# Optimization experiments

Measured on AMD Instinct MI355X. Metric: run time of the kernel, lower is better.

The kernel has to match this reference:

```python
import jax, jax.numpy as jnp
import numpy as np

BSZ, SEQ, EMBED = 2, 4096, 1024
NUM_HEADS = 16
HEAD_DIM = EMBED // NUM_HEADS
WINDOW = 256  # attention_window[layer_id]


def setup_inputs() -> dict:
    key = jax.random.key(0)
    ks = jax.random.split(key, 7)
    s = 1.0 / np.sqrt(EMBED)
    return {
        "hidden_states": jax.random.normal(ks[0], (BSZ, SEQ, EMBED), jnp.float32),
        "Wq": jax.random.normal(ks[1], (EMBED, EMBED), jnp.float32) * s,
        "bq": jnp.zeros((EMBED,), jnp.float32),
        "Wk": jax.random.normal(ks[2], (EMBED, EMBED), jnp.float32) * s,
        "bk": jnp.zeros((EMBED,), jnp.float32),
        "Wv": jax.random.normal(ks[3], (EMBED, EMBED), jnp.float32) * s,
        "bv": jnp.zeros((EMBED,), jnp.float32),
    }


def _blocks3(x, nb, w):
    # x: [b, s + 2w, h, d] -> [b, nb, 3w, h, d]; block c sees key blocks c-1, c, c+1
    b = x.shape[0]
    xb = x.reshape(b, nb + 2, w, NUM_HEADS, HEAD_DIM)
    return jnp.concatenate([xb[:, i:i + nb] for i in range(3)], axis=2)


def reference(hidden_states, Wq, bq, Wk, bk, Wv, bv):
    b, s, e = hidden_states.shape
    w = WINDOW
    nb = s // w
    q = (hidden_states @ Wq + bq) * (1.0 / np.sqrt(HEAD_DIM))
    k = hidden_states @ Wk + bk
    v = hidden_states @ Wv + bv
    q = q.reshape(b, nb, w, NUM_HEADS, HEAD_DIM)
    k = k.reshape(b, s, NUM_HEADS, HEAD_DIM)
    v = v.reshape(b, s, NUM_HEADS, HEAD_DIM)
    pad = ((0, 0), (w, w), (0, 0), (0, 0))
    kb = _blocks3(jnp.pad(k, pad), nb, w)  # [b, nb, 3w, h, d]
    vb = _blocks3(jnp.pad(v, pad), nb, w)
    # banded scores: query x in block n attends keys at global pos n*w - w + y
    scores = jnp.einsum('bnxhd,bnyhd->bnhxy', q, kb)  # [b, nb, h, w, 3w]
    x_idx = jnp.arange(w)
    y_idx = jnp.arange(3 * w)
    band = jnp.abs(y_idx[None, :] - x_idx[:, None] - w) <= w  # [w, 3w]
    kpos = jnp.arange(nb)[:, None] * w - w + y_idx[None, :]   # [nb, 3w]
    inb = (kpos >= 0) & (kpos < s)
    mask = band[None, :, :] & inb[:, None, :]                 # [nb, w, 3w]
    scores = jnp.where(mask[None, :, None, :, :], scores, -jnp.inf)
    probs = jax.nn.softmax(scores.astype(jnp.float32), axis=-1).astype(v.dtype)
    attn = jnp.einsum('bnhxy,bnyhd->bnxhd', probs, vb)        # [b, nb, w, h, d]
    return attn.reshape(b, s, e)
```

## Files before the change

### kernel.cpp

```cpp
#include <hip/hip_runtime.h>
#include <stdint.h>

#define SEQ    4096
#define EMBED  1024
#define NHEAD  16
#define HDIM   64
#define WIN    256
#define BSZ    2
#define M_TOT  (BSZ * SEQ)
#define N_QKV  3072
#define N_QK   2048
#define K_DIM  1024
#define LOG2E  1.4426950408889634f

typedef __attribute__((ext_vector_type(8))) __bf16 bf16x8;
typedef __attribute__((ext_vector_type(4))) float  f32x4;

__device__ __forceinline__ unsigned short f2bf(float f) {
  union { float f; unsigned int u; } c; c.f = f;
  unsigned int u = c.u;
  unsigned int r = (u + 0x7FFFu + ((u >> 16) & 1u)) >> 16;
  return (unsigned short)r;
}

__device__ __forceinline__ unsigned int cvt_pk_bf16(float lo, float hi) {
  unsigned int r;
  asm("v_cvt_pk_bf16_f32 %0, %1, %2" : "=v"(r) : "v"(lo), "v"(hi));
  return r;
}

__device__ __forceinline__ void gl2lds16(const void* g, void* l) {
  __builtin_amdgcn_global_load_lds((const __attribute__((address_space(1))) void*)g,
                                   (__attribute__((address_space(3))) void*)l, 16, 0, 0);
}

__global__ __launch_bounds__(256) void cvt_all(const float* __restrict__ in,
                                               unsigned short* __restrict__ out,
                                               const float* __restrict__ Wq,
                                               const float* __restrict__ Wk,
                                               const float* __restrict__ Wv,
                                               unsigned short* __restrict__ Wt) {
  __shared__ float t[32][33];
  int tid = threadIdx.x;
  if (blockIdx.x < 8192) {
    int i = (blockIdx.x * 256 + tid) * 4;
    float4 v = *(const float4*)(in + i);
    ushort4 o;
    o.x = f2bf(v.x); o.y = f2bf(v.y); o.z = f2bf(v.z); o.w = f2bf(v.w);
    *(ushort4*)(out + i) = o;
  } else {
    int wb = blockIdx.x - 8192;
    int z  = wb >> 10;
    int rem = wb & 1023;
    int kb = (rem & 31) * 32, nb = (rem >> 5) * 32;
    const float* W = (z == 0) ? Wq : (z == 1) ? Wk : Wv;
    int tx = tid & 31, ty = tid >> 5;
    for (int it = 0; it < 4; ++it) {
      int k = kb + ty + it * 8;
      t[ty + it * 8][tx] = W[(size_t)k * 1024 + nb + tx];
    }
    __syncthreads();
    for (int it = 0; it < 4; ++it) {
      int n = nb + ty + it * 8;
      Wt[(size_t)(z * 1024 + n) * 1024 + kb + tx] = f2bf(t[tx][ty + it * 8]);
    }
  }
}

__global__ __launch_bounds__(512, 2) void qkv_gemm(const unsigned short* __restrict__ A,
                                                   const unsigned short* __restrict__ Bt,
                                                   const float* __restrict__ bq,
                                                   const float* __restrict__ bk,
                                                   const float* __restrict__ bv,
                                                   unsigned short* __restrict__ C,
                                                   unsigned short* __restrict__ Vt) {
  __shared__ unsigned short As[2][128 * 64];
  __shared__ unsigned short Bs[2][384 * 64];
  int tid  = threadIdx.x;
  int lane = tid & 63, wave = tid >> 6;
  int ln   = lane & 15, quad = lane >> 4;
  int flat = blockIdx.y * 8 + blockIdx.x;
  int swz  = (flat & 7) * 64 + (flat >> 3);
  int m0 = (swz >> 3) * 128, n0 = (swz & 7) * 384;
  int wy = wave >> 2, wx = wave & 3;
  f32x4 acc[4][6];
#pragma unroll
  for (int i = 0; i < 4; ++i)
#pragma unroll
    for (int j = 0; j < 6; ++j) acc[i][j] = (f32x4){0.f, 0.f, 0.f, 0.f};

  int c8 = tid & 7;

#define STG_A(buf, kt)                                                           \
  do {                                                                           \
    _Pragma("unroll")                                                            \
    for (int s = 0; s < 2; ++s) {                                                \
      int r = s * 64 + (tid >> 3); int cg = c8 ^ (r & 7);                        \
      gl2lds16(A + (size_t)(m0 + r) * K_DIM + (size_t)(kt) * 64 + cg * 8,        \
               &As[buf][r * 64 + c8 * 8]);                                       \
    }                                                                            \
  } while (0)
#define STG_B(buf, jreg, kt)                                                     \
  do {                                                                           \
    _Pragma("unroll")                                                            \
    for (int s = 0; s < 2; ++s) {                                                \
      int r = s * 64 + (tid >> 3); int gr = (jreg) * 128 + r;                    \
      int cg = c8 ^ (gr & 7);                                                    \
      gl2lds16(Bt + (size_t)(n0 + gr) * K_DIM + (size_t)(kt) * 64 + cg * 8,      \
               &Bs[buf][gr * 64 + c8 * 8]);                                      \
    }                                                                            \
  } while (0)

  STG_A(0, 0); STG_B(0, 0, 0); STG_B(0, 1, 0); STG_B(0, 2, 0);
  STG_B(1, 0, 1); STG_B(1, 1, 1); STG_B(1, 2, 1);
  asm volatile("s_waitcnt vmcnt(6)" ::: "memory");
  __builtin_amdgcn_s_barrier();

  int aBase = wy * 64, bBase = wx * 96;

#pragma unroll 1
  for (int t = 0; t < 16; ++t) {
    int cur = t & 1;
    const unsigned short* as = As[cur];
    const unsigned short* bs = Bs[cur];
    bf16x8 af[4][2], bf01[2][2], bf23[2][2], bf45[2][2];

#pragma unroll
    for (int i2 = 0; i2 < 4; ++i2) {
      int row = aBase + i2 * 16 + ln;
#pragma unroll
      for (int ks = 0; ks < 2; ++ks) {
        int c = (ks * 4 + quad) ^ (row & 7);
        af[i2][ks] = *(const bf16x8*)&as[row * 64 + c * 8];
      }
    }
#pragma unroll
    for (int j2 = 0; j2 < 2; ++j2) {
      int row = bBase + j2 * 16 + ln;
#pragma unroll
      for (int ks = 0; ks < 2; ++ks) {
        int c = (ks * 4 + quad) ^ (row & 7);
        bf01[j2][ks] = *(const bf16x8*)&bs[row * 64 + c * 8];
      }
    }
    if (t < 15) STG_A(cur ^ 1, t + 1);
    __builtin_amdgcn_s_barrier();
    __builtin_amdgcn_s_setprio(1);
#pragma unroll
    for (int ks = 0; ks < 2; ++ks)
#pragma unroll
      for (int i2 = 0; i2 < 4; ++i2)
#pragma unroll
        for (int j2 = 0; j2 < 2; ++j2)
          acc[i2][j2] = __builtin_amdgcn_mfma_f32_16x16x32_bf16(af[i2][ks], bf01[j2][ks], acc[i2][j2], 0, 0, 0);
    __builtin_amdgcn_s_setprio(0);
    __builtin_amdgcn_s_barrier();

#pragma unroll
    for (int j2 = 0; j2 < 2; ++j2) {
      int row = bBase + 32 + j2 * 16 + ln;
#pragma unroll
      for (int ks = 0; ks < 2; ++ks) {
        int c = (ks * 4 + quad) ^ (row & 7);
        bf23[j2][ks] = *(const bf16x8*)&bs[row * 64 + c * 8];
      }
    }
    __builtin_amdgcn_s_barrier();
    __builtin_amdgcn_s_setprio(1);
#pragma unroll
    for (int ks = 0; ks < 2; ++ks)
#pragma unroll
      for (int i2 = 0; i2 < 4; ++i2)
#pragma unroll
        for (int j2 = 0; j2 < 2; ++j2)
          acc[i2][2 + j2] = __builtin_amdgcn_mfma_f32_16x16x32_bf16(af[i2][ks], bf23[j2][ks], acc[i2][2 + j2], 0, 0, 0);
    __builtin_amdgcn_s_setprio(0);
    __builtin_amdgcn_s_barrier();

#pragma unroll
    for (int j2 = 0; j2 < 2; ++j2) {
      int row = bBase + 64 + j2 * 16 + ln;
#pragma unroll
      for (int ks = 0; ks < 2; ++ks) {
        int c = (ks * 4 + quad) ^ (row & 7);
        bf45[j2][ks] = *(const bf16x8*)&bs[row * 64 + c * 8];
      }
    }
    __builtin_amdgcn_s_barrier();
    if (t < 14) { STG_B(cur, 0, t + 2); STG_B(cur, 1, t + 2); STG_B(cur, 2, t + 2); }
    __builtin_amdgcn_s_setprio(1);
#pragma unroll
    for (int ks = 0; ks < 2; ++ks)
#pragma unroll
      for (int i2 = 0; i2 < 4; ++i2)
#pragma unroll
        for (int j2 = 0; j2 < 2; ++j2)
          acc[i2][4 + j2] = __builtin_amdgcn_mfma_f32_16x16x32_bf16(af[i2][ks], bf45[j2][ks], acc[i2][4 + j2], 0, 0, 0);
    __builtin_amdgcn_s_setprio(0);
    if (t < 14) asm volatile("s_waitcnt vmcnt(6)" ::: "memory");
    else        asm volatile("s_waitcnt vmcnt(0)" ::: "memory");
    __builtin_amdgcn_s_barrier();
  }
#undef STG_A
#undef STG_B

#pragma unroll
  for (int j = 0; j < 6; ++j) {
    int n = n0 + wx * 96 + j * 16 + ln;
    if (n < N_QK) {
      float bias, scl;
      if (n < 1024) { bias = bq[n];        scl = 0.125f * LOG2E; }
      else          { bias = bk[n - 1024]; scl = 1.f; }
#pragma unroll
      for (int i = 0; i < 4; ++i) {
        int mb = m0 + wy * 64 + i * 16 + quad * 4;
#pragma unroll
        for (int r = 0; r < 4; ++r) {
          float v = (acc[i][j][r] + bias) * scl;
          C[(size_t)(mb + r) * N_QK + n] = f2bf(v);
        }
      }
    } else {
      int hd = n - 2048;
      float bias = bv[hd];
#pragma unroll
      for (int i = 0; i < 4; ++i) {
        int mb  = m0 + wy * 64 + i * 16 + quad * 4;
        int bb  = mb >> 12;
        int pos = mb & (SEQ - 1);
        ushort4 pk;
        pk.x = f2bf(acc[i][j][0] + bias);
        pk.y = f2bf(acc[i][j][1] + bias);
        pk.z = f2bf(acc[i][j][2] + bias);
        pk.w = f2bf(acc[i][j][3] + bias);
        *(ushort4*)&Vt[((size_t)bb * (NHEAD * HDIM) + hd) * SEQ + pos] = pk;
      }
    }
  }
}

__global__ __launch_bounds__(256) void attn(const unsigned short* __restrict__ qk,
                                            const unsigned short* __restrict__ vtg,
                                            float* __restrict__ out) {
  __shared__ unsigned short Kl[64 * 72];
  __shared__ unsigned short Vl[64 * 72];
  int tid  = threadIdx.x;
  int lane = tid & 63, wave = tid >> 6;
  int ln   = lane & 15, quad = lane >> 4;
  int bx = blockIdx.x;
  int lx = ((bx & 7) << 3) | (bx >> 3);
  int q0 = lx * 64, head = blockIdx.y, b = blockIdx.z;
  size_t baseRow = (size_t)b * SEQ;
  const unsigned short* kptr = qk + 1024;
  const unsigned short* vrow = vtg + ((size_t)(b * NHEAD + head) * HDIM) * SEQ;

  int sy = tid >> 3, sc = tid & 7;
  const unsigned short* kbase = kptr + (baseRow + sy) * (size_t)N_QK + head * HDIM + sc * 8;
  const unsigned short* vbase = vrow + (size_t)sy * SEQ + sc * 8;

  bf16x8 qf[2];
  {
    size_t ro = (baseRow + q0 + wave * 16 + ln) * (size_t)N_QK + head * HDIM + quad * 8;
    qf[0] = *(const bf16x8*)&qk[ro];
    qf[1] = *(const bf16x8*)&qk[ro + 32];
  }

  float l_st = 0.f;
  f32x4 o_acc[4];
  for (int dt = 0; dt < 4; ++dt) o_acc[dt] = (f32x4){0.f, 0.f, 0.f, 0.f};

  int lo = (q0 >= 256) ? 0 : (256 - q0) / 64;
  int hi = (SEQ + 256 - q0) / 64; if (hi > 9) hi = 9;

  uint4 pk0, pk1, pv0, pv1;
#define PREFETCH(KT)                                                        \
  {                                                                         \
    pk0 = *(const uint4*)&kbase[(size_t)(KT) * N_QK];                       \
    pk1 = *(const uint4*)&kbase[(size_t)((KT) + 32) * N_QK];                \
    pv0 = *(const uint4*)&vbase[(KT)];                                      \
    pv1 = *(const uint4*)&vbase[(size_t)32 * SEQ + (KT)];                   \
  }

  PREFETCH(q0 - 256 + lo * 64);

  int srcA = ((lane & 16) << 1) | ln;
  int srcB = srcA + 16;
  bool hiQ = (lane & 32) != 0;

  for (int t = lo; t < hi; ++t) {
    int kt = q0 - 256 + t * 64;
    __syncthreads();
    *(uint4*)&Kl[sy * 72 + sc * 8]        = pk0;
    *(uint4*)&Kl[(sy + 32) * 72 + sc * 8] = pk1;
    *(uint4*)&Vl[sy * 72 + sc * 8]        = pv0;
    *(uint4*)&Vl[(sy + 32) * 72 + sc * 8] = pv1;
    __syncthreads();

    if (t + 1 < hi) { PREFETCH(kt + 64); }

    f32x4 s[4];
    __builtin_amdgcn_s_setprio(1);
    for (int nt = 0; nt < 4; ++nt) {
      bf16x8 kf0 = *(const bf16x8*)&Kl[(nt * 16 + ln) * 72 + quad * 8];
      bf16x8 kf1 = *(const bf16x8*)&Kl[(nt * 16 + ln) * 72 + 32 + quad * 8];
      f32x4 z = (f32x4){0.f, 0.f, 0.f, 0.f};
      z = __builtin_amdgcn_mfma_f32_16x16x32_bf16(kf0, qf[0], z, 0, 0, 0);
      z = __builtin_amdgcn_mfma_f32_16x16x32_bf16(kf1, qf[1], z, 0, 0, 0);
      s[nt] = z;
    }
    __builtin_amdgcn_s_setprio(0);

    if (t == 0 || t == 8) {
      int qq = q0 + wave * 16 + ln;
      for (int nt = 0; nt < 4; ++nt) {
        int kb = kt + nt * 16 + quad * 4 - qq;
        for (int r = 0; r < 4; ++r) {
          int dd = kb + r;
          if (dd < -WIN || dd > WIN) s[nt][r] = -INFINITY;
        }
      }
    }

    float rs = 0.f;
    for (int nt = 0; nt < 4; ++nt)
      for (int r = 0; r < 4; ++r) {
        float p = exp2f(s[nt][r]);
        s[nt][r] = p;
        rs += p;
      }
    l_st += rs;

    unsigned int p01[4], p23[4];
    for (int nt = 0; nt < 4; ++nt) {
      p01[nt] = cvt_pk_bf16(s[nt][0], s[nt][1]);
      p23[nt] = cvt_pk_bf16(s[nt][2], s[nt][3]);
    }

    for (int ks = 0; ks < 2; ++ks) {
      int ntA = 2 * ks, ntB = 2 * ks + 1;
      unsigned int a0 = (unsigned int)__shfl((int)p01[ntA], srcA);
      unsigned int a1 = (unsigned int)__shfl((int)p23[ntA], srcA);
      unsigned int a2 = (unsigned int)__shfl((int)p01[ntA], srcB);
      unsigned int a3 = (unsigned int)__shfl((int)p23[ntA], srcB);
      unsigned int b0 = (unsigned int)__shfl((int)p01[ntB], srcA);
      unsigned int b1 = (unsigned int)__shfl((int)p23[ntB], srcA);
      unsigned int b2 = (unsigned int)__shfl((int)p01[ntB], srcB);
      unsigned int b3 = (unsigned int)__shfl((int)p23[ntB], srcB);
      union { uint4 u; bf16x8 v; } pf;
      pf.u.x = hiQ ? b0 : a0;
      pf.u.y = hiQ ? b1 : a1;
      pf.u.z = hiQ ? b2 : a2;
      pf.u.w = hiQ ? b3 : a3;
      __builtin_amdgcn_s_setprio(1);
      for (int dt = 0; dt < 4; ++dt) {
        bf16x8 vf = *(const bf16x8*)&Vl[(dt * 16 + ln) * 72 + ks * 32 + quad * 8];
        o_acc[dt] = __builtin_amdgcn_mfma_f32_16x16x32_bf16(vf, pf.v, o_acc[dt], 0, 0, 0);
      }
      __builtin_amdgcn_s_setprio(0);
    }
  }

  float l = l_st;
  l += __shfl_xor(l, 16);
  l += __shfl_xor(l, 32);
  float inv = 1.0f / l;
  int qpos = q0 + wave * 16 + ln;
  float* ob = out + (baseRow + qpos) * (size_t)EMBED + head * HDIM + quad * 4;
  for (int dt = 0; dt < 4; ++dt) {
    float4 v;
    v.x = o_acc[dt][0] * inv;
    v.y = o_acc[dt][1] * inv;
    v.z = o_acc[dt][2] * inv;
    v.w = o_acc[dt][3] * inv;
    *(float4*)(ob + dt * 16) = v;
  }
#undef PREFETCH
}

extern "C" void kernel_launch(void* const* d_in, const int* in_sizes, int n_in,
                              void* d_out, int out_size, void* d_ws, size_t ws_size,
                              hipStream_t stream) {
  const float* h  = (const float*)d_in[0];
  const float* Wq = (const float*)d_in[1];
  const float* bq = (const float*)d_in[2];
  const float* Wk = (const float*)d_in[3];
  const float* bk = (const float*)d_in[4];
  const float* Wv = (const float*)d_in[5];
  const float* bv = (const float*)d_in[6];
  float* out = (float*)d_out;

  unsigned short* h_bf  = (unsigned short*)d_ws;
  unsigned short* wt_bf = h_bf + (size_t)M_TOT * K_DIM;
  unsigned short* qk    = wt_bf + (size_t)N_QKV * K_DIM;
  unsigned short* vtg   = qk + (size_t)M_TOT * N_QK;

  cvt_all<<<8192 + 3072, 256, 0, stream>>>(h, h_bf, Wq, Wk, Wv, wt_bf);
  qkv_gemm<<<dim3(8, 64), 512, 0, stream>>>(h_bf, wt_bf, bq, bk, bv, qk, vtg);
  attn<<<dim3(SEQ / 64, NHEAD, BSZ), 256, 0, stream>>>(qk, vtg, out);
}
```

Measured before the change: 207.6 us.

## Double attention query tile per block to reuse K/V tiles across 128 queries

Each attention block now handles 128 queries instead of 64. Every wave computes two 16-row query groups against the same K/V fragments held in shared memory, which amortises K/V global and LDS loads over twice the work. Key tiles per block grow from 9 to 10, the boundary masking covers the first two and last two tiles, and the grid is halved. The cost is roughly double the accumulator and score registers, which may lower occupancy, and fewer blocks in the grid.

```diff
diff --git a/kernel.cpp b/kernel.cpp
--- a/kernel.cpp
+++ b/kernel.cpp
@@ -248,8 +248,8 @@
   int lane = tid & 63, wave = tid >> 6;
   int ln   = lane & 15, quad = lane >> 4;
   int bx = blockIdx.x;
-  int lx = ((bx & 7) << 3) | (bx >> 3);
-  int q0 = lx * 64, head = blockIdx.y, b = blockIdx.z;
+  int lx = ((bx & 7) << 2) | (bx >> 3);
+  int q0 = lx * 128, head = blockIdx.y, b = blockIdx.z;
   size_t baseRow = (size_t)b * SEQ;
   const unsigned short* kptr = qk + 1024;
   const unsigned short* vrow = vtg + ((size_t)(b * NHEAD + head) * HDIM) * SEQ;
@@ -258,19 +258,22 @@
   const unsigned short* kbase = kptr + (baseRow + sy) * (size_t)N_QK + head * HDIM + sc * 8;
   const unsigned short* vbase = vrow + (size_t)sy * SEQ + sc * 8;
 
-  bf16x8 qf[2];
+  bf16x8 qfA[2], qfB[2];
   {
-    size_t ro = (baseRow + q0 + wave * 16 + ln) * (size_t)N_QK + head * HDIM + quad * 8;
-    qf[0] = *(const bf16x8*)&qk[ro];
-    qf[1] = *(const bf16x8*)&qk[ro + 32];
-  }
-
-  float l_st = 0.f;
-  f32x4 o_acc[4];
-  for (int dt = 0; dt < 4; ++dt) o_acc[dt] = (f32x4){0.f, 0.f, 0.f, 0.f};
+    size_t roA = (baseRow + q0 + wave * 32 + ln) * (size_t)N_QK + head * HDIM + quad * 8;
+    qfA[0] = *(const bf16x8*)&qk[roA];
+    qfA[1] = *(const bf16x8*)&qk[roA + 32];
+    size_t roB = roA + 16 * (size_t)N_QK;
+    qfB[0] = *(const bf16x8*)&qk[roB];
+    qfB[1] = *(const bf16x8*)&qk[roB + 32];
+  }
+
+  float lA = 0.f, lB = 0.f;
+  f32x4 oA[4], oB[4];
+  for (int dt = 0; dt < 4; ++dt) { oA[dt] = (f32x4){0.f,0.f,0.f,0.f}; oB[dt] = (f32x4){0.f,0.f,0.f,0.f}; }
 
   int lo = (q0 >= 256) ? 0 : (256 - q0) / 64;
-  int hi = (SEQ + 256 - q0) / 64; if (hi > 9) hi = 9;
+  int hi = (SEQ + 256 - q0) / 64; if (hi > 10) hi = 10;
 
   uint4 pk0, pk1, pv0, pv1;
 #define PREFETCH(KT)                                                        \
@@ -298,81 +301,105 @@
 
     if (t + 1 < hi) { PREFETCH(kt + 64); }
 
-    f32x4 s[4];
+    f32x4 sA[4], sB[4];
     __builtin_amdgcn_s_setprio(1);
     for (int nt = 0; nt < 4; ++nt) {
       bf16x8 kf0 = *(const bf16x8*)&Kl[(nt * 16 + ln) * 72 + quad * 8];
       bf16x8 kf1 = *(const bf16x8*)&Kl[(nt * 16 + ln) * 72 + 32 + quad * 8];
-      f32x4 z = (f32x4){0.f, 0.f, 0.f, 0.f};
-      z = __builtin_amdgcn_mfma_f32_16x16x32_bf16(kf0, qf[0], z, 0, 0, 0);
-      z = __builtin_amdgcn_mfma_f32_16x16x32_bf16(kf1, qf[1], z, 0, 0, 0);
-      s[nt] = z;
+      f32x4 zA = (f32x4){0.f, 0.f, 0.f, 0.f};
+      zA = __builtin_amdgcn_mfma_f32_16x16x32_bf16(kf0, qfA[0], zA, 0, 0, 0);
+      zA = __builtin_amdgcn_mfma_f32_16x16x32_bf16(kf1, qfA[1], zA, 0, 0, 0);
+      sA[nt] = zA;
+      f32x4 zB = (f32x4){0.f, 0.f, 0.f, 0.f};
+      zB = __builtin_amdgcn_mfma_f32_16x16x32_bf16(kf0, qfB[0], zB, 0, 0, 0);
+      zB = __builtin_amdgcn_mfma_f32_16x16x32_bf16(kf1, qfB[1], zB, 0, 0, 0);
+      sB[nt] = zB;
     }
     __builtin_amdgcn_s_setprio(0);
 
-    if (t == 0 || t == 8) {
-      int qq = q0 + wave * 16 + ln;
+    if (t < 2 || t >= 8) {
+      int qqA = q0 + wave * 32 + ln;
+      int qqB = qqA + 16;
       for (int nt = 0; nt < 4; ++nt) {
-        int kb = kt + nt * 16 + quad * 4 - qq;
+        int kb = kt + nt * 16 + quad * 4;
         for (int r = 0; r < 4; ++r) {
-          int dd = kb + r;
-          if (dd < -WIN || dd > WIN) s[nt][r] = -INFINITY;
+          int dA = kb + r - qqA;
+          int dB = kb + r - qqB;
+          if (dA < -WIN || dA > WIN) sA[nt][r] = -INFINITY;
+          if (dB < -WIN || dB > WIN) sB[nt][r] = -INFINITY;
         }
       }
     }
 
-    float rs = 0.f;
+    float rsA = 0.f, rsB = 0.f;
     for (int nt = 0; nt < 4; ++nt)
       for (int r = 0; r < 4; ++r) {
-        float p = exp2f(s[nt][r]);
-        s[nt][r] = p;
-        rs += p;
-      }
-    l_st += rs;
-
-    unsigned int p01[4], p23[4];
+        float pA = exp2f(sA[nt][r]); sA[nt][r] = pA; rsA += pA;
+        float pB = exp2f(sB[nt][r]); sB[nt][r] = pB; rsB += pB;
+      }
+    lA += rsA; lB += rsB;
+
+    unsigned int pA01[4], pA23[4], pB01[4], pB23[4];
     for (int nt = 0; nt < 4; ++nt) {
-      p01[nt] = cvt_pk_bf16(s[nt][0], s[nt][1]);
-      p23[nt] = cvt_pk_bf16(s[nt][2], s[nt][3]);
+      pA01[nt] = cvt_pk_bf16(sA[nt][0], sA[nt][1]);
+      pA23[nt] = cvt_pk_bf16(sA[nt][2], sA[nt][3]);
+      pB01[nt] = cvt_pk_bf16(sB[nt][0], sB[nt][1]);
+      pB23[nt] = cvt_pk_bf16(sB[nt][2], sB[nt][3]);
     }
 
     for (int ks = 0; ks < 2; ++ks) {
       int ntA = 2 * ks, ntB = 2 * ks + 1;
-      unsigned int a0 = (unsigned int)__shfl((int)p01[ntA], srcA);
-      unsigned int a1 = (unsigned int)__shfl((int)p23[ntA], srcA);
-      unsigned int a2 = (unsigned int)__shfl((int)p01[ntA], srcB);
-      unsigned int a3 = (unsigned int)__shfl((int)p23[ntA], srcB);
-      unsigned int b0 = (unsigned int)__shfl((int)p01[ntB], srcA);
-      unsigned int b1 = (unsigned int)__shfl((int)p23[ntB], srcA);
-      unsigned int b2 = (unsigned int)__shfl((int)p01[ntB], srcB);
-      unsigned int b3 = (unsigned int)__shfl((int)p23[ntB], srcB);
-      union { uint4 u; bf16x8 v; } pf;
-      pf.u.x = hiQ ? b0 : a0;
-      pf.u.y = hiQ ? b1 : a1;
-      pf.u.z = hiQ ? b2 : a2;
-      pf.u.w = hiQ ? b3 : a3;
+      unsigned int a0 = (unsigned int)__shfl((int)pA01[ntA], srcA);
+      unsigned int a1 = (unsigned int)__shfl((int)pA23[ntA], srcA);
+      unsigned int a2 = (unsigned int)__shfl((int)pA01[ntA], srcB);
+      unsigned int a3 = (unsigned int)__shfl((int)pA23[ntA], srcB);
+      unsigned int a4 = (unsigned int)__shfl((int)pA01[ntB], srcA);
+      unsigned int a5 = (unsigned int)__shfl((int)pA23[ntB], srcA);
+      unsigned int a6 = (unsigned int)__shfl((int)pA01[ntB], srcB);
+      unsigned int a7 = (unsigned int)__shfl((int)pA23[ntB], srcB);
+      union { uint4 u; bf16x8 v; } pfA;
+      pfA.u.x = hiQ ? a4 : a0;
+      pfA.u.y = hiQ ? a5 : a1;
+      pfA.u.z = hiQ ? a6 : a2;
+      pfA.u.w = hiQ ? a7 : a3;
+      unsigned int b0 = (unsigned int)__shfl((int)pB01[ntA], srcA);
+      unsigned int b1 = (unsigned int)__shfl((int)pB23[ntA], srcA);
+      unsigned int b2 = (unsigned int)__shfl((int)pB01[ntA], srcB);
+      unsigned int b3 = (unsigned int)__shfl((int)pB23[ntA], srcB);
+      unsigned int b4 = (unsigned int)__shfl((int)pB01[ntB], srcA);
+      unsigned int b5 = (unsigned int)__shfl((int)pB23[ntB], srcA);
+      unsigned int b6 = (unsigned int)__shfl((int)pB01[ntB], srcB);
+      unsigned int b7 = (unsigned int)__shfl((int)pB23[ntB], srcB);
+      union { uint4 u; bf16x8 v; } pfB;
+      pfB.u.x = hiQ ? b4 : b0;
+      pfB.u.y = hiQ ? b5 : b1;
+      pfB.u.z = hiQ ? b6 : b2;
+      pfB.u.w = hiQ ? b7 : b3;
       __builtin_amdgcn_s_setprio(1);
       for (int dt = 0; dt < 4; ++dt) {
         bf16x8 vf = *(const bf16x8*)&Vl[(dt * 16 + ln) * 72 + ks * 32 + quad * 8];
-        o_acc[dt] = __builtin_amdgcn_mfma_f32_16x16x32_bf16(vf, pf.v, o_acc[dt], 0, 0, 0);
+        oA[dt] = __builtin_amdgcn_mfma_f32_16x16x32_bf16(vf, pfA.v, oA[dt], 0, 0, 0);
+        oB[dt] = __builtin_amdgcn_mfma_f32_16x16x32_bf16(vf, pfB.v, oB[dt], 0, 0, 0);
       }
       __builtin_amdgcn_s_setprio(0);
     }
   }
 
-  float l = l_st;
-  l += __shfl_xor(l, 16);
-  l += __shfl_xor(l, 32);
-  float inv = 1.0f / l;
-  int qpos = q0 + wave * 16 + ln;
-  float* ob = out + (baseRow + qpos) * (size_t)EMBED + head * HDIM + quad * 4;
+  float la = lA, lb = lB;
+  la += __shfl_xor(la, 16); la += __shfl_xor(la, 32);
+  lb += __shfl_xor(lb, 16); lb += __shfl_xor(lb, 32);
+  float invA = 1.0f / la, invB = 1.0f / lb;
+  int qposA = q0 + wave * 32 + ln;
+  float* obA = out + (baseRow + qposA) * (size_t)EMBED + head * HDIM + quad * 4;
+  float* obB = obA + 16 * (size_t)EMBED;
   for (int dt = 0; dt < 4; ++dt) {
-    float4 v;
-    v.x = o_acc[dt][0] * inv;
-    v.y = o_acc[dt][1] * inv;
-    v.z = o_acc[dt][2] * inv;
-    v.w = o_acc[dt][3] * inv;
-    *(float4*)(ob + dt * 16) = v;
+    float4 vA, vB;
+    vA.x = oA[dt][0] * invA; vA.y = oA[dt][1] * invA;
+    vA.z = oA[dt][2] * invA; vA.w = oA[dt][3] * invA;
+    *(float4*)(obA + dt * 16) = vA;
+    vB.x = oB[dt][0] * invB; vB.y = oB[dt][1] * invB;
+    vB.z = oB[dt][2] * invB; vB.w = oB[dt][3] * invB;
+    *(float4*)(obB + dt * 16) = vB;
   }
 #undef PREFETCH
 }
@@ -396,5 +423,5 @@
 
   cvt_all<<<8192 + 3072, 256, 0, stream>>>(h, h_bf, Wq, Wk, Wv, wt_bf);
   qkv_gemm<<<dim3(8, 64), 512, 0, stream>>>(h_bf, wt_bf, bq, bk, bv, qk, vtg);
-  attn<<<dim3(SEQ / 64, NHEAD, BSZ), 256, 0, stream>>>(qk, vtg, out);
-}
+  attn<<<dim3(SEQ / 128, NHEAD, BSZ), 256, 0, stream>>>(qk, vtg, out);
+}
```

Measured after the change: 212.3 us. +2.3%, slower.

## Load K/V MFMA fragments directly from global memory, dropping LDS staging

Applied to the files above, without the earlier changes.

The attention kernel no longer stages K and V tiles in shared memory with block-wide barriers and register prefetch. Each wave now loads its own K and V MFMA operand fragments straight from global memory at the start of every key tile, and loops are explicitly unrolled. This removes the LDS writes, both __syncthreads per tile and the LDS reads. In exchange the four waves each fetch the same K/V data (4x redundant global/L2 traffic), there is no software prefetch across tiles, and V reads are strided rows that rely on cache hits.

```diff
diff --git a/kernel.cpp b/kernel.cpp
--- a/kernel.cpp
+++ b/kernel.cpp
@@ -242,8 +242,6 @@
 __global__ __launch_bounds__(256) void attn(const unsigned short* __restrict__ qk,
                                             const unsigned short* __restrict__ vtg,
                                             float* __restrict__ out) {
-  __shared__ unsigned short Kl[64 * 72];
-  __shared__ unsigned short Vl[64 * 72];
   int tid  = threadIdx.x;
   int lane = tid & 63, wave = tid >> 6;
   int ln   = lane & 15, quad = lane >> 4;
@@ -251,12 +249,8 @@
   int lx = ((bx & 7) << 3) | (bx >> 3);
   int q0 = lx * 64, head = blockIdx.y, b = blockIdx.z;
   size_t baseRow = (size_t)b * SEQ;
-  const unsigned short* kptr = qk + 1024;
-  const unsigned short* vrow = vtg + ((size_t)(b * NHEAD + head) * HDIM) * SEQ;
-
-  int sy = tid >> 3, sc = tid & 7;
-  const unsigned short* kbase = kptr + (baseRow + sy) * (size_t)N_QK + head * HDIM + sc * 8;
-  const unsigned short* vbase = vrow + (size_t)sy * SEQ + sc * 8;
+  const unsigned short* kfp = qk + 1024 + head * HDIM + quad * 8;
+  const unsigned short* vrow = vtg + ((size_t)(b * NHEAD + head) * HDIM) * SEQ + quad * 8;
 
   bf16x8 qf[2];
   {
@@ -272,48 +266,44 @@
   int lo = (q0 >= 256) ? 0 : (256 - q0) / 64;
   int hi = (SEQ + 256 - q0) / 64; if (hi > 9) hi = 9;
 
-  uint4 pk0, pk1, pv0, pv1;
-#define PREFETCH(KT)                                                        \
-  {                                                                         \
-    pk0 = *(const uint4*)&kbase[(size_t)(KT) * N_QK];                       \
-    pk1 = *(const uint4*)&kbase[(size_t)((KT) + 32) * N_QK];                \
-    pv0 = *(const uint4*)&vbase[(KT)];                                      \
-    pv1 = *(const uint4*)&vbase[(size_t)32 * SEQ + (KT)];                   \
-  }
-
-  PREFETCH(q0 - 256 + lo * 64);
-
   int srcA = ((lane & 16) << 1) | ln;
   int srcB = srcA + 16;
   bool hiQ = (lane & 32) != 0;
 
   for (int t = lo; t < hi; ++t) {
     int kt = q0 - 256 + t * 64;
-    __syncthreads();
-    *(uint4*)&Kl[sy * 72 + sc * 8]        = pk0;
-    *(uint4*)&Kl[(sy + 32) * 72 + sc * 8] = pk1;
-    *(uint4*)&Vl[sy * 72 + sc * 8]        = pv0;
-    *(uint4*)&Vl[(sy + 32) * 72 + sc * 8] = pv1;
-    __syncthreads();
-
-    if (t + 1 < hi) { PREFETCH(kt + 64); }
+
+    bf16x8 kf0[4], kf1[4];
+#pragma unroll
+    for (int nt = 0; nt < 4; ++nt) {
+      size_t kr = (baseRow + (size_t)(kt + nt * 16 + ln)) * (size_t)N_QK;
+      kf0[nt] = *(const bf16x8*)&kfp[kr];
+      kf1[nt] = *(const bf16x8*)&kfp[kr + 32];
+    }
+    bf16x8 vf[2][4];
+#pragma unroll
+    for (int ks = 0; ks < 2; ++ks)
+#pragma unroll
+      for (int dt = 0; dt < 4; ++dt)
+        vf[ks][dt] = *(const bf16x8*)&vrow[(size_t)(dt * 16 + ln) * SEQ + kt + ks * 32];
 
     f32x4 s[4];
     __builtin_amdgcn_s_setprio(1);
+#pragma unroll
     for (int nt = 0; nt < 4; ++nt) {
-      bf16x8 kf0 = *(const bf16x8*)&Kl[(nt * 16 + ln) * 72 + quad * 8];
-      bf16x8 kf1 = *(const bf16x8*)&Kl[(nt * 16 + ln) * 72 + 32 + quad * 8];
       f32x4 z = (f32x4){0.f, 0.f, 0.f, 0.f};
-      z = __builtin_amdgcn_mfma_f32_16x16x32_bf16(kf0, qf[0], z, 0, 0, 0);
-      z = __builtin_amdgcn_mfma_f32_16x16x32_bf16(kf1, qf[1], z, 0, 0, 0);
+      z = __builtin_amdgcn_mfma_f32_16x16x32_bf16(kf0[nt], qf[0], z, 0, 0, 0);
+      z = __builtin_amdgcn_mfma_f32_16x16x32_bf16(kf1[nt], qf[1], z, 0, 0, 0);
       s[nt] = z;
     }
     __builtin_amdgcn_s_setprio(0);
 
     if (t == 0 || t == 8) {
       int qq = q0 + wave * 16 + ln;
+#pragma unroll
       for (int nt = 0; nt < 4; ++nt) {
         int kb = kt + nt * 16 + quad * 4 - qq;
+#pragma unroll
         for (int r = 0; r < 4; ++r) {
           int dd = kb + r;
           if (dd < -WIN || dd > WIN) s[nt][r] = -INFINITY;
@@ -322,7 +312,9 @@
     }
 
     float rs = 0.f;
+#pragma unroll
     for (int nt = 0; nt < 4; ++nt)
+#pragma unroll
       for (int r = 0; r < 4; ++r) {
         float p = exp2f(s[nt][r]);
         s[nt][r] = p;
@@ -331,11 +323,13 @@
     l_st += rs;
 
     unsigned int p01[4], p23[4];
+#pragma unroll
     for (int nt = 0; nt < 4; ++nt) {
       p01[nt] = cvt_pk_bf16(s[nt][0], s[nt][1]);
       p23[nt] = cvt_pk_bf16(s[nt][2], s[nt][3]);
     }
 
+#pragma unroll
     for (int ks = 0; ks < 2; ++ks) {
       int ntA = 2 * ks, ntB = 2 * ks + 1;
       unsigned int a0 = (unsigned int)__shfl((int)p01[ntA], srcA);
@@ -352,10 +346,9 @@
       pf.u.z = hiQ ? b2 : a2;
       pf.u.w = hiQ ? b3 : a3;
       __builtin_amdgcn_s_setprio(1);
-      for (int dt = 0; dt < 4; ++dt) {
-        bf16x8 vf = *(const bf16x8*)&Vl[(dt * 16 + ln) * 72 + ks * 32 + quad * 8];
-        o_acc[dt] = __builtin_amdgcn_mfma_f32_16x16x32_bf16(vf, pf.v, o_acc[dt], 0, 0, 0);
-      }
+#pragma unroll
+      for (int dt = 0; dt < 4; ++dt)
+        o_acc[dt] = __builtin_amdgcn_mfma_f32_16x16x32_bf16(vf[ks][dt], pf.v, o_acc[dt], 0, 0, 0);
       __builtin_amdgcn_s_setprio(0);
     }
   }
@@ -374,7 +367,6 @@
     v.w = o_acc[dt][3] * inv;
     *(float4*)(ob + dt * 16) = v;
   }
-#undef PREFETCH
 }
 
 extern "C" void kernel_launch(void* const* d_in, const int* in_sizes, int n_in,
```

Result: slower. 290.3 us (+39.9%).
